# Kernel tuning notes

Hardware: AMD Instinct MI355X
Metric: run time of the kernel (lower is better)

Reference implementation:

```python
import jax, jax.numpy as jnp
import numpy as np

D_MODEL = 1024
N_HEAD = 16
D_K = D_MODEL // N_HEAD


def setup_inputs() -> dict:
    key = jax.random.key(0)
    ks = jax.random.split(key, 11)
    B, T = 2, 2048
    s = 1.0 / np.sqrt(D_MODEL)
    return {
        "q": jax.random.normal(ks[0], (B, T, D_MODEL), jnp.float32),
        "k": jax.random.normal(ks[1], (B, T, D_MODEL), jnp.float32),
        "v": jax.random.normal(ks[2], (B, T, D_MODEL), jnp.float32),
        "w_q": jax.random.normal(ks[3], (D_MODEL, D_MODEL), jnp.float32) * s,
        "b_q": jax.random.normal(ks[4], (D_MODEL,), jnp.float32) * 0.01,
        "w_k": jax.random.normal(ks[5], (D_MODEL, D_MODEL), jnp.float32) * s,
        "b_k": jax.random.normal(ks[6], (D_MODEL,), jnp.float32) * 0.01,
        "w_v": jax.random.normal(ks[7], (D_MODEL, D_MODEL), jnp.float32) * s,
        "b_v": jax.random.normal(ks[8], (D_MODEL,), jnp.float32) * 0.01,
        "w_o": jax.random.normal(ks[9], (D_MODEL, D_MODEL), jnp.float32) * s,
        "b_o": jax.random.normal(ks[10], (D_MODEL,), jnp.float32) * 0.01,
    }


def reference(q, k, v, w_q, b_q, w_k, b_k, w_v, b_v, w_o, b_o):
    B, T, _ = q.shape
    # QKV projections -> [B, H, T, d_k]
    def proj(x, w, b):
        return (jnp.einsum('btd,de->bte', x, w) + b).reshape(B, T, N_HEAD, D_K).transpose(0, 2, 1, 3)
    qh = proj(q, w_q, b_q)
    kh = proj(k, w_k, b_k)
    vh = proj(v, w_v, b_v)
    scale = jnp.float32(1.0 / np.sqrt(D_K))
    scores = jnp.einsum('bhqd,bhkd->bhqk', qh, kh) * scale  # [B,H,T,T]
    attn = jax.nn.softmax(scores, axis=-1)
    # dropout is identity in eval mode
    out = jnp.einsum('bhqk,bhkd->bhqd', attn, vh)  # [B,H,T,d_k]
    out = out.transpose(0, 2, 1, 3).reshape(B, T, N_HEAD * D_K)
    return jnp.einsum('btd,de->bte', out, w_o) + b_o
```

## Files before the change

kernel.cpp:

```cpp
#include <hip/hip_runtime.h>
#include <stdint.h>

#define DEVI static __device__ __forceinline__

typedef float f32x4 __attribute__((ext_vector_type(4)));
typedef float f32x16 __attribute__((ext_vector_type(16)));
typedef short s16x8 __attribute__((ext_vector_type(8)));
typedef unsigned short u16x4 __attribute__((ext_vector_type(4)));
typedef uint32_t u32x2 __attribute__((ext_vector_type(2)));
typedef uint32_t u32x4 __attribute__((ext_vector_type(4)));

DEVI unsigned short f2bf(float f) {
  union { float f; uint32_t u; } v; v.f = f;
  uint32_t u = v.u;
  return (unsigned short)((u + 0x7fffu + ((u >> 16) & 1u)) >> 16);
}

DEVI uint32_t cvtpk(float lo, float hi) {
  uint32_t r;
  asm("v_cvt_pk_bf16_f32 %0, %1, %2" : "=v"(r) : "v"(lo), "v"(hi));
  return r;
}

DEVI void pl32swap(uint32_t& a, uint32_t& b) {
#if __has_builtin(__builtin_amdgcn_permlane32_swap)
  u32x2 r = __builtin_amdgcn_permlane32_swap(a, b, false, false);
  a = r[0]; b = r[1];
#else
  asm("v_permlane32_swap_b32 %0, %1" : "+v"(a), "+v"(b));
#endif
}

DEVI float swap_half(float x, int hi) {
  uint32_t a = __float_as_uint(x), b = a;
  pl32swap(a, b);
  return hi ? __uint_as_float(a) : __uint_as_float(b);
}

DEVI void g2l16(const void* g, void* l) {
  __builtin_amdgcn_global_load_lds(
      (const __attribute__((address_space(1))) void*)g,
      (__attribute__((address_space(3))) void*)l, 16, 0, 0);
}

DEVI float vmax16(const f32x16& v) {
  float a = fmaxf(fmaxf(v[0], v[1]), fmaxf(v[2], v[3]));
  float b = fmaxf(fmaxf(v[4], v[5]), fmaxf(v[6], v[7]));
  float c = fmaxf(fmaxf(v[8], v[9]), fmaxf(v[10], v[11]));
  float d = fmaxf(fmaxf(v[12], v[13]), fmaxf(v[14], v[15]));
  return fmaxf(fmaxf(a, b), fmaxf(c, d));
}

DEVI float vsum16(const f32x16& v) {
  float a = (v[0] + v[1]) + (v[2] + v[3]);
  float b = (v[4] + v[5]) + (v[6] + v[7]);
  float c = (v[8] + v[9]) + (v[10] + v[11]);
  float d = (v[12] + v[13]) + (v[14] + v[15]);
  return (a + b) + (c + d);
}

__global__ __launch_bounds__(256) void k_cvt3(const float* __restrict__ q,
                                              const float* __restrict__ k,
                                              const float* __restrict__ v,
                                              unsigned short* __restrict__ out) {
  const int y = blockIdx.y;
  const float* in = y == 0 ? q : y == 1 ? k : v;
  unsigned short* o = out + (size_t)y * 4194304;
  int idx = blockIdx.x * blockDim.x + threadIdx.x;
  int stride = gridDim.x * blockDim.x;
  for (int i = idx * 4; i < 4194304; i += stride * 4) {
    f32x4 x = *(const f32x4*)(in + i);
    u16x4 r;
    for (int j = 0; j < 4; ++j) r[j] = f2bf(x[j]);
    *(u16x4*)(o + i) = r;
  }
}

__global__ __launch_bounds__(256) void k_wt4(const float* w0, const float* w1,
                                             const float* w2, const float* w3,
                                             unsigned short* t0, unsigned short* t1,
                                             unsigned short* t2, unsigned short* t3) {
  const int z = blockIdx.z;
  const float* w = z == 0 ? w0 : z == 1 ? w1 : z == 2 ? w2 : w3;
  unsigned short* wt = z == 0 ? t0 : z == 1 ? t1 : z == 2 ? t2 : t3;
  __shared__ float tile[32][33];
  const int tx = threadIdx.x, ty = threadIdx.y;
  const int n0 = blockIdx.x * 32, k0 = blockIdx.y * 32;
  for (int j = 0; j < 4; ++j)
    tile[ty + j * 8][tx] = w[(size_t)(k0 + ty + j * 8) * 1024 + n0 + tx];
  __syncthreads();
  for (int j = 0; j < 4; ++j)
    wt[(size_t)(n0 + ty + j * 8) * 1024 + k0 + tx] = f2bf(tile[tx][ty + j * 8]);
}

__global__ __launch_bounds__(256) void k_gemm_multi(
    const unsigned short* A0, const unsigned short* A1, const unsigned short* A2,
    const unsigned short* B0, const unsigned short* B1, const unsigned short* B2,
    const float* c0, const float* c1, const float* c2,
    void* o0, void* o1, void* o2, int mode0) {
  constexpr int K = 1024;
  const int z = blockIdx.y;
  const unsigned short* A = z == 0 ? A0 : z == 1 ? A1 : A2;
  const unsigned short* Bt = z == 0 ? B0 : z == 1 ? B1 : B2;
  const float* bias = z == 0 ? c0 : z == 1 ? c1 : c2;
  void* outp = z == 0 ? o0 : z == 1 ? o1 : o2;
  const int MODE = mode0 + z;

  __shared__ __align__(16) unsigned short As[128 * 64];
  __shared__ __align__(16) unsigned short Bs[64 * 64];
  const int tid = threadIdx.x;
  const int lane = tid & 63, w = tid >> 6;
  const int g = lane >> 4, c = lane & 15;
  const int wgid = (blockIdx.x & 7) * 64 + (blockIdx.x >> 3);
  const int bm = wgid >> 4, bn = wgid & 15;
  const int m0 = bm * 128, n0 = bn * 64;
  const int wr = w >> 1, wc = w & 1;
  f32x4 acc[4][2] = {};

  for (int kt = 0; kt < 16; ++kt) {
    const int k0 = kt * 64;
    __syncthreads();
#pragma unroll
    for (int it = 0; it < 4; ++it) {
      int e = it * 256 + tid;
      int row = e >> 3, cwp = (e & 7) ^ (row & 7);
      g2l16(A + (size_t)(m0 + row) * K + k0 + cwp * 8,
            (char*)As + (it * 256 + (w << 6)) * 16);
    }
#pragma unroll
    for (int it = 0; it < 2; ++it) {
      int e = it * 256 + tid;
      int row = e >> 3, cwp = (e & 7) ^ (row & 7);
      g2l16(Bt + (size_t)(n0 + row) * K + k0 + cwp * 8,
            (char*)Bs + (it * 256 + (w << 6)) * 16);
    }
    __syncthreads();
    for (int kk = 0; kk < 2; ++kk) {
      s16x8 af[4], bfr[2];
      for (int mi = 0; mi < 4; ++mi) {
        int row = wr * 64 + mi * 16 + c;
        int ch = (kk * 4 + g) ^ (row & 7);
        af[mi] = *(const s16x8*)((const char*)As + row * 128 + ch * 16);
      }
      for (int ni = 0; ni < 2; ++ni) {
        int row = wc * 32 + ni * 16 + c;
        int ch = (kk * 4 + g) ^ (row & 7);
        bfr[ni] = *(const s16x8*)((const char*)Bs + row * 128 + ch * 16);
      }
      for (int mi = 0; mi < 4; ++mi)
        for (int ni = 0; ni < 2; ++ni)
          acc[mi][ni] = __builtin_amdgcn_mfma_f32_16x16x32_bf16(
              af[mi], bfr[ni], acc[mi][ni], 0, 0, 0);
    }
  }

  if (MODE == 0 || MODE == 1) {
    unsigned short* out = (unsigned short*)outp;
    const float scale = (MODE == 0) ? 0.1803368801111204f : 1.0f;
    for (int mi = 0; mi < 4; ++mi)
      for (int ni = 0; ni < 2; ++ni) {
        int row = m0 + wr * 64 + mi * 16 + g * 4;
        int col = n0 + wc * 32 + ni * 16 + c;
        float bb = bias[col];
        for (int r = 0; r < 4; ++r)
          out[(size_t)(row + r) * 1024 + col] = f2bf((acc[mi][ni][r] + bb) * scale);
      }
  } else if (MODE == 2) {
    unsigned short* vt = (unsigned short*)outp;
    const int bq = m0 >> 11, t0 = m0 & 2047;
    for (int mi = 0; mi < 4; ++mi)
      for (int ni = 0; ni < 2; ++ni) {
        int rowb = wr * 64 + mi * 16 + g * 4;
        int coll = wc * 32 + ni * 16 + c;
        float bb = bias[n0 + coll];
        u16x4 pk;
        for (int r = 0; r < 4; ++r) pk[r] = f2bf(acc[mi][ni][r] + bb);
        *(u16x4*)(vt + (size_t)(bq * 1024 + n0 + coll) * 2048 + t0 + rowb) = pk;
      }
  } else {
    float* out = (float*)outp;
    for (int mi = 0; mi < 4; ++mi)
      for (int ni = 0; ni < 2; ++ni) {
        int row = m0 + wr * 64 + mi * 16 + g * 4;
        int col = n0 + wc * 32 + ni * 16 + c;
        float bb = bias[col];
        for (int r = 0; r < 4; ++r)
          out[(size_t)(row + r) * 1024 + col] = acc[mi][ni][r] + bb;
      }
  }
}

__global__ __launch_bounds__(128) void k_attn(const unsigned short* __restrict__ Qp,
                                              const unsigned short* __restrict__ Kp,
                                              const unsigned short* __restrict__ Vt,
                                              unsigned short* __restrict__ Att) {
  __shared__ __align__(16) unsigned short Ks[2][4096];
  __shared__ __align__(16) unsigned short Vs[2][4096];
  const int tid = threadIdx.x;
  const int lane = tid & 63, w = tid >> 6;
  const int l31 = lane & 31, hi = lane >> 5;
  const int blk = (blockIdx.x & 7) * 128 + (blockIdx.x >> 3);
  const int qt = blk & 31, bh = blk >> 5;
  const int b = bh >> 4, h = bh & 15;
  const int m0 = qt * 64 + w * 32;
  const size_t qkBase = (size_t)b * 2048 * 1024 + (size_t)h * 64;
  const size_t vtBase = ((size_t)b * 1024 + h * 64) * 2048;

  const unsigned short* qrow = Qp + qkBase + (size_t)(m0 + l31) * 1024;
  s16x8 bq[4];
#pragma unroll
  for (int s = 0; s < 4; ++s)
    bq[s] = *(const s16x8*)(qrow + s * 16 + hi * 8);

  const int srow = tid >> 1, half = tid & 1;
  const unsigned short* kg = Kp + qkBase + (size_t)srow * 1024 + half * 32;
  const unsigned short* vg = Vt + vtBase + (size_t)srow * 2048 + half * 32;
  int wof[4];
#pragma unroll
  for (int j = 0; j < 4; ++j)
    wof[j] = srow * 128 + (((half * 4 + j) ^ (srow & 7)) * 16);

  float m_run = -1e30f, l_run = 0.f;
  f32x16 o0 = {}, o1 = {};

  {
    s16x8 k0 = *(const s16x8*)(kg), k1 = *(const s16x8*)(kg + 8);
    s16x8 k2 = *(const s16x8*)(kg + 16), k3 = *(const s16x8*)(kg + 24);
    s16x8 v0 = *(const s16x8*)(vg), v1 = *(const s16x8*)(vg + 8);
    s16x8 v2 = *(const s16x8*)(vg + 16), v3 = *(const s16x8*)(vg + 24);
    *(s16x8*)((char*)&Ks[0][0] + wof[0]) = k0;
    *(s16x8*)((char*)&Ks[0][0] + wof[1]) = k1;
    *(s16x8*)((char*)&Ks[0][0] + wof[2]) = k2;
    *(s16x8*)((char*)&Ks[0][0] + wof[3]) = k3;
    *(s16x8*)((char*)&Vs[0][0] + wof[0]) = v0;
    *(s16x8*)((char*)&Vs[0][0] + wof[1]) = v1;
    *(s16x8*)((char*)&Vs[0][0] + wof[2]) = v2;
    *(s16x8*)((char*)&Vs[0][0] + wof[3]) = v3;
  }
  __syncthreads();

  const int rch = l31 & 7;

#pragma unroll 1
  for (int t = 0; t < 32; ++t) {
    const int cur = t & 1;
    s16x8 k0, k1, k2, k3, v0, v1, v2, v3;
    if (t < 31) {
      const unsigned short* kgt = kg + (size_t)(t + 1) * 65536;
      const unsigned short* vgt = vg + (t + 1) * 64;
      k0 = *(const s16x8*)(kgt);      k1 = *(const s16x8*)(kgt + 8);
      k2 = *(const s16x8*)(kgt + 16); k3 = *(const s16x8*)(kgt + 24);
      v0 = *(const s16x8*)(vgt);      v1 = *(const s16x8*)(vgt + 8);
      v2 = *(const s16x8*)(vgt + 16); v3 = *(const s16x8*)(vgt + 24);
    }
    const char* ks = (const char*)&Ks[cur][0];
    const char* vs = (const char*)&Vs[cur][0];

    f32x16 s0 = {}, s1 = {};
    __builtin_amdgcn_s_setprio(1);
#pragma unroll
    for (int ds = 0; ds < 4; ++ds) {
      int ch = (2 * ds + hi) ^ rch;
      s16x8 a0 = *(const s16x8*)(ks + l31 * 128 + ch * 16);
      s16x8 a1 = *(const s16x8*)(ks + (32 + l31) * 128 + ch * 16);
      s0 = __builtin_amdgcn_mfma_f32_32x32x16_bf16(a0, bq[ds], s0, 0, 0, 0);
      s1 = __builtin_amdgcn_mfma_f32_32x32x16_bf16(a1, bq[ds], s1, 0, 0, 0);
    }
    __builtin_amdgcn_s_setprio(0);

    float tm = fmaxf(vmax16(s0), vmax16(s1));
    tm = fmaxf(tm, swap_half(tm, hi));
    if (!__all(tm - m_run <= 8.0f)) {
      float mt = fmaxf(m_run, tm);
      float al = exp2f(m_run - mt);
      l_run *= al;
#pragma unroll
      for (int j = 0; j < 16; ++j) { o0[j] *= al; o1[j] *= al; }
      m_run = mt;
    }
#pragma unroll
    for (int j = 0; j < 16; ++j) s0[j] = exp2f(s0[j] - m_run);
#pragma unroll
    for (int j = 0; j < 16; ++j) s1[j] = exp2f(s1[j] - m_run);
    l_run += vsum16(s0) + vsum16(s1);

    s16x8 pf[4];
    {
      uint32_t w0 = cvtpk(s0[0], s0[1]), w1 = cvtpk(s0[2], s0[3]);
      uint32_t w2 = cvtpk(s0[4], s0[5]), w3 = cvtpk(s0[6], s0[7]);
      uint32_t w4 = cvtpk(s0[8], s0[9]), w5 = cvtpk(s0[10], s0[11]);
      uint32_t w6 = cvtpk(s0[12], s0[13]), w7 = cvtpk(s0[14], s0[15]);
      pl32swap(w0, w2); pl32swap(w1, w3); pl32swap(w4, w6); pl32swap(w5, w7);
      u32x4 f0 = {w0, w1, w2, w3}, f1 = {w4, w5, w6, w7};
      pf[0] = *(s16x8*)&f0;
      pf[1] = *(s16x8*)&f1;
    }
    {
      uint32_t w0 = cvtpk(s1[0], s1[1]), w1 = cvtpk(s1[2], s1[3]);
      uint32_t w2 = cvtpk(s1[4], s1[5]), w3 = cvtpk(s1[6], s1[7]);
      uint32_t w4 = cvtpk(s1[8], s1[9]), w5 = cvtpk(s1[10], s1[11]);
      uint32_t w6 = cvtpk(s1[12], s1[13]), w7 = cvtpk(s1[14], s1[15]);
      pl32swap(w0, w2); pl32swap(w1, w3); pl32swap(w4, w6); pl32swap(w5, w7);
      u32x4 f0 = {w0, w1, w2, w3}, f1 = {w4, w5, w6, w7};
      pf[2] = *(s16x8*)&f0;
      pf[3] = *(s16x8*)&f1;
    }

    __builtin_amdgcn_s_setprio(1);
#pragma unroll
    for (int ksp = 0; ksp < 4; ++ksp) {
      int ch = (2 * ksp + hi) ^ rch;
      s16x8 a0 = *(const s16x8*)(vs + l31 * 128 + ch * 16);
      s16x8 a1 = *(const s16x8*)(vs + (32 + l31) * 128 + ch * 16);
      o0 = __builtin_amdgcn_mfma_f32_32x32x16_bf16(a0, pf[ksp], o0, 0, 0, 0);
      o1 = __builtin_amdgcn_mfma_f32_32x32x16_bf16(a1, pf[ksp], o1, 0, 0, 0);
    }
    __builtin_amdgcn_s_setprio(0);

    if (t < 31) {
      const int nb = cur ^ 1;
      *(s16x8*)((char*)&Ks[nb][0] + wof[0]) = k0;
      *(s16x8*)((char*)&Ks[nb][0] + wof[1]) = k1;
      *(s16x8*)((char*)&Ks[nb][0] + wof[2]) = k2;
      *(s16x8*)((char*)&Ks[nb][0] + wof[3]) = k3;
      *(s16x8*)((char*)&Vs[nb][0] + wof[0]) = v0;
      *(s16x8*)((char*)&Vs[nb][0] + wof[1]) = v1;
      *(s16x8*)((char*)&Vs[nb][0] + wof[2]) = v2;
      *(s16x8*)((char*)&Vs[nb][0] + wof[3]) = v3;
    }
    __syncthreads();
  }

  float lt = l_run + swap_half(l_run, hi);
  float inv = 1.0f / lt;
  unsigned short* arow = Att + ((size_t)b * 2048 + m0 + l31) * 1024 + h * 64;
#pragma unroll
  for (int dblk = 0; dblk < 2; ++dblk) {
#pragma unroll
    for (int rq = 0; rq < 4; ++rq) {
      float e0 = (dblk ? o1[rq * 4 + 0] : o0[rq * 4 + 0]) * inv;
      float e1 = (dblk ? o1[rq * 4 + 1] : o0[rq * 4 + 1]) * inv;
      float e2 = (dblk ? o1[rq * 4 + 2] : o0[rq * 4 + 2]) * inv;
      float e3 = (dblk ? o1[rq * 4 + 3] : o0[rq * 4 + 3]) * inv;
      u32x2 pk;
      pk[0] = cvtpk(e0, e1);
      pk[1] = cvtpk(e2, e3);
      *(u32x2*)(arow + dblk * 32 + 8 * rq + 4 * hi) = pk;
    }
  }
}

extern "C" void kernel_launch(void* const* d_in, const int* in_sizes, int n_in,
                              void* d_out, int out_size, void* d_ws, size_t ws_size,
                              hipStream_t stream) {
  const float* q = (const float*)d_in[0];
  const float* k = (const float*)d_in[1];
  const float* v = (const float*)d_in[2];
  const float* w_q = (const float*)d_in[3];
  const float* b_q = (const float*)d_in[4];
  const float* w_k = (const float*)d_in[5];
  const float* b_k = (const float*)d_in[6];
  const float* w_v = (const float*)d_in[7];
  const float* b_v = (const float*)d_in[8];
  const float* w_o = (const float*)d_in[9];
  const float* b_o = (const float*)d_in[10];

  unsigned short* s = (unsigned short*)d_ws;
  unsigned short* qbf = s;
  unsigned short* kbf = s + 4194304;
  unsigned short* vbf = s + 8388608;
  unsigned short* wqT = s + 12582912;
  unsigned short* wkT = s + 13631488;
  unsigned short* wvT = s + 14680064;
  unsigned short* woT = s + 15728640;
  unsigned short* Qp  = s + 16777216;
  unsigned short* Kp  = s + 20971520;
  unsigned short* Vt  = s + 25165824;
  unsigned short* Att = qbf;

  k_cvt3<<<dim3(1024, 3), 256, 0, stream>>>(q, k, v, qbf);

  k_wt4<<<dim3(32, 32, 4), dim3(32, 8), 0, stream>>>(w_q, w_k, w_v, w_o,
                                                     wqT, wkT, wvT, woT);

  k_gemm_multi<<<dim3(512, 3), 256, 0, stream>>>(
      qbf, kbf, vbf, wqT, wkT, wvT, b_q, b_k, b_v,
      (void*)Qp, (void*)Kp, (void*)Vt, 0);

  k_attn<<<1024, 128, 0, stream>>>(Qp, Kp, Vt, Att);

  k_gemm_multi<<<dim3(512, 1), 256, 0, stream>>>(
      Att, Att, Att, woT, woT, woT, b_o, b_o, b_o,
      d_out, d_out, d_out, 3);
}
```

Before: 147.3 us.

## Split attention over two key halves with 128-query blocks and a combine kernel

The attention kernel now uses 256-thread blocks covering 128 queries, so four waves share each K/V tile loaded into LDS. Each block processes only half of the key sequence. Per-half normalized outputs and (max, sum) statistics go to workspace, and a new combine kernel merges them with softmax rescaling. This is meant to improve K/V reuse per block and keep the grid size unchanged. In exchange it adds an extra launch, extra global traffic for the bf16 partial outputs, and a second bf16 rounding step. Softmax exponentials also switch to the native exp2 builtin.

```diff
diff --git a/kernel.cpp b/kernel.cpp
--- a/kernel.cpp
+++ b/kernel.cpp
@@ -16,10 +16,24 @@
   return (unsigned short)((u + 0x7fffu + ((u >> 16) & 1u)) >> 16);
 }
 
+DEVI float bf2f(unsigned short u) {
+  union { uint32_t u; float f; } v;
+  v.u = ((uint32_t)u) << 16;
+  return v.f;
+}
+
 DEVI uint32_t cvtpk(float lo, float hi) {
   uint32_t r;
   asm("v_cvt_pk_bf16_f32 %0, %1, %2" : "=v"(r) : "v"(lo), "v"(hi));
   return r;
+}
+
+DEVI float fexp2(float x) {
+#if __has_builtin(__builtin_amdgcn_exp2f)
+  return __builtin_amdgcn_exp2f(x);
+#else
+  return exp2f(x);
+#endif
 }
 
 DEVI void pl32swap(uint32_t& a, uint32_t& b) {
@@ -190,19 +204,21 @@
   }
 }
 
-__global__ __launch_bounds__(128) void k_attn(const unsigned short* __restrict__ Qp,
+__global__ __launch_bounds__(256) void k_attn(const unsigned short* __restrict__ Qp,
                                               const unsigned short* __restrict__ Kp,
                                               const unsigned short* __restrict__ Vt,
-                                              unsigned short* __restrict__ Att) {
+                                              unsigned short* __restrict__ Po0,
+                                              unsigned short* __restrict__ Po1,
+                                              float2* __restrict__ ml) {
   __shared__ __align__(16) unsigned short Ks[2][4096];
   __shared__ __align__(16) unsigned short Vs[2][4096];
   const int tid = threadIdx.x;
   const int lane = tid & 63, w = tid >> 6;
   const int l31 = lane & 31, hi = lane >> 5;
   const int blk = (blockIdx.x & 7) * 128 + (blockIdx.x >> 3);
-  const int qt = blk & 31, bh = blk >> 5;
+  const int half = blk & 1, qt = (blk >> 1) & 15, bh = blk >> 5;
   const int b = bh >> 4, h = bh & 15;
-  const int m0 = qt * 64 + w * 32;
+  const int m0 = qt * 128 + w * 32;
   const size_t qkBase = (size_t)b * 2048 * 1024 + (size_t)h * 64;
   const size_t vtBase = ((size_t)b * 1024 + h * 64) * 2048;
 
@@ -212,46 +228,40 @@
   for (int s = 0; s < 4; ++s)
     bq[s] = *(const s16x8*)(qrow + s * 16 + hi * 8);
 
-  const int srow = tid >> 1, half = tid & 1;
-  const unsigned short* kg = Kp + qkBase + (size_t)srow * 1024 + half * 32;
-  const unsigned short* vg = Vt + vtBase + (size_t)srow * 2048 + half * 32;
-  int wof[4];
-#pragma unroll
-  for (int j = 0; j < 4; ++j)
-    wof[j] = srow * 128 + (((half * 4 + j) ^ (srow & 7)) * 16);
+  const int srow = tid >> 2, c4 = tid & 3;
+  const unsigned short* kg = Kp + qkBase + (size_t)srow * 1024 + c4 * 16 +
+                             (size_t)half * 1048576;
+  const unsigned short* vg = Vt + vtBase + (size_t)srow * 2048 + c4 * 16 +
+                             half * 1024;
+  int wof[2];
+#pragma unroll
+  for (int j = 0; j < 2; ++j)
+    wof[j] = srow * 128 + (((c4 * 2 + j) ^ (srow & 7)) * 16);
 
   float m_run = -1e30f, l_run = 0.f;
   f32x16 o0 = {}, o1 = {};
 
   {
     s16x8 k0 = *(const s16x8*)(kg), k1 = *(const s16x8*)(kg + 8);
-    s16x8 k2 = *(const s16x8*)(kg + 16), k3 = *(const s16x8*)(kg + 24);
     s16x8 v0 = *(const s16x8*)(vg), v1 = *(const s16x8*)(vg + 8);
-    s16x8 v2 = *(const s16x8*)(vg + 16), v3 = *(const s16x8*)(vg + 24);
     *(s16x8*)((char*)&Ks[0][0] + wof[0]) = k0;
     *(s16x8*)((char*)&Ks[0][0] + wof[1]) = k1;
-    *(s16x8*)((char*)&Ks[0][0] + wof[2]) = k2;
-    *(s16x8*)((char*)&Ks[0][0] + wof[3]) = k3;
     *(s16x8*)((char*)&Vs[0][0] + wof[0]) = v0;
     *(s16x8*)((char*)&Vs[0][0] + wof[1]) = v1;
-    *(s16x8*)((char*)&Vs[0][0] + wof[2]) = v2;
-    *(s16x8*)((char*)&Vs[0][0] + wof[3]) = v3;
   }
   __syncthreads();
 
   const int rch = l31 & 7;
 
 #pragma unroll 1
-  for (int t = 0; t < 32; ++t) {
+  for (int t = 0; t < 16; ++t) {
     const int cur = t & 1;
-    s16x8 k0, k1, k2, k3, v0, v1, v2, v3;
-    if (t < 31) {
+    s16x8 k0, k1, v0, v1;
+    if (t < 15) {
       const unsigned short* kgt = kg + (size_t)(t + 1) * 65536;
       const unsigned short* vgt = vg + (t + 1) * 64;
-      k0 = *(const s16x8*)(kgt);      k1 = *(const s16x8*)(kgt + 8);
-      k2 = *(const s16x8*)(kgt + 16); k3 = *(const s16x8*)(kgt + 24);
-      v0 = *(const s16x8*)(vgt);      v1 = *(const s16x8*)(vgt + 8);
-      v2 = *(const s16x8*)(vgt + 16); v3 = *(const s16x8*)(vgt + 24);
+      k0 = *(const s16x8*)(kgt); k1 = *(const s16x8*)(kgt + 8);
+      v0 = *(const s16x8*)(vgt); v1 = *(const s16x8*)(vgt + 8);
     }
     const char* ks = (const char*)&Ks[cur][0];
     const char* vs = (const char*)&Vs[cur][0];
@@ -272,16 +282,16 @@
     tm = fmaxf(tm, swap_half(tm, hi));
     if (!__all(tm - m_run <= 8.0f)) {
       float mt = fmaxf(m_run, tm);
-      float al = exp2f(m_run - mt);
+      float al = fexp2(m_run - mt);
       l_run *= al;
 #pragma unroll
       for (int j = 0; j < 16; ++j) { o0[j] *= al; o1[j] *= al; }
       m_run = mt;
     }
 #pragma unroll
-    for (int j = 0; j < 16; ++j) s0[j] = exp2f(s0[j] - m_run);
-#pragma unroll
-    for (int j = 0; j < 16; ++j) s1[j] = exp2f(s1[j] - m_run);
+    for (int j = 0; j < 16; ++j) s0[j] = fexp2(s0[j] - m_run);
+#pragma unroll
+    for (int j = 0; j < 16; ++j) s1[j] = fexp2(s1[j] - m_run);
     l_run += vsum16(s0) + vsum16(s1);
 
     s16x8 pf[4];
@@ -317,23 +327,20 @@
     }
     __builtin_amdgcn_s_setprio(0);
 
-    if (t < 31) {
+    if (t < 15) {
       const int nb = cur ^ 1;
       *(s16x8*)((char*)&Ks[nb][0] + wof[0]) = k0;
       *(s16x8*)((char*)&Ks[nb][0] + wof[1]) = k1;
-      *(s16x8*)((char*)&Ks[nb][0] + wof[2]) = k2;
-      *(s16x8*)((char*)&Ks[nb][0] + wof[3]) = k3;
       *(s16x8*)((char*)&Vs[nb][0] + wof[0]) = v0;
       *(s16x8*)((char*)&Vs[nb][0] + wof[1]) = v1;
-      *(s16x8*)((char*)&Vs[nb][0] + wof[2]) = v2;
-      *(s16x8*)((char*)&Vs[nb][0] + wof[3]) = v3;
     }
     __syncthreads();
   }
 
   float lt = l_run + swap_half(l_run, hi);
   float inv = 1.0f / lt;
-  unsigned short* arow = Att + ((size_t)b * 2048 + m0 + l31) * 1024 + h * 64;
+  unsigned short* Po = half ? Po1 : Po0;
+  unsigned short* arow = Po + ((size_t)b * 2048 + m0 + l31) * 1024 + h * 64;
 #pragma unroll
   for (int dblk = 0; dblk < 2; ++dblk) {
 #pragma unroll
@@ -348,6 +355,36 @@
       *(u32x2*)(arow + dblk * 32 + 8 * rq + 4 * hi) = pk;
     }
   }
+  if (hi == 0) {
+    int qid = ((b << 4) + h) * 2048 + m0 + l31;
+    ml[half * 65536 + qid] = {m_run, lt};
+  }
+}
+
+__global__ __launch_bounds__(256) void k_comb(const unsigned short* __restrict__ Po0,
+                                              const unsigned short* __restrict__ Po1,
+                                              const float2* __restrict__ ml,
+                                              unsigned short* __restrict__ Att) {
+  int idx = blockIdx.x * 256 + threadIdx.x;
+  int base = idx * 8;
+  int qrow = base >> 10, col = base & 1023;
+  int h = col >> 6, b = qrow >> 11, t = qrow & 2047;
+  int qid = ((b << 4) + h) * 2048 + t;
+  float2 p0 = ml[qid], p1 = ml[65536 + qid];
+  float ms = fmaxf(p0.x, p1.x);
+  float a0 = fexp2(p0.x - ms) * p0.y, a1 = fexp2(p1.x - ms) * p1.y;
+  float inv = 1.0f / (a0 + a1);
+  float w0 = a0 * inv, w1 = a1 * inv;
+  s16x8 v0 = *(const s16x8*)(Po0 + base);
+  s16x8 v1 = *(const s16x8*)(Po1 + base);
+  u32x4 pk;
+#pragma unroll
+  for (int j = 0; j < 4; ++j) {
+    float e0 = w0 * bf2f((unsigned short)v0[2 * j]) + w1 * bf2f((unsigned short)v1[2 * j]);
+    float e1 = w0 * bf2f((unsigned short)v0[2 * j + 1]) + w1 * bf2f((unsigned short)v1[2 * j + 1]);
+    pk[j] = cvtpk(e0, e1);
+  }
+  *(u32x4*)(Att + base) = pk;
 }
 
 extern "C" void kernel_launch(void* const* d_in, const int* in_sizes, int n_in,
@@ -376,7 +413,10 @@
   unsigned short* Qp  = s + 16777216;
   unsigned short* Kp  = s + 20971520;
   unsigned short* Vt  = s + 25165824;
-  unsigned short* Att = qbf;
+  unsigned short* Po0 = qbf;
+  unsigned short* Po1 = kbf;
+  unsigned short* Att = vbf;
+  float2* ml = (float2*)wqT;
 
   k_cvt3<<<dim3(1024, 3), 256, 0, stream>>>(q, k, v, qbf);
 
@@ -387,7 +427,9 @@
       qbf, kbf, vbf, wqT, wkT, wvT, b_q, b_k, b_v,
       (void*)Qp, (void*)Kp, (void*)Vt, 0);
 
-  k_attn<<<1024, 128, 0, stream>>>(Qp, Kp, Vt, Att);
+  k_attn<<<1024, 256, 0, stream>>>(Qp, Kp, Vt, Po0, Po1, ml);
+
+  k_comb<<<2048, 256, 0, stream>>>(Po0, Po1, ml, Att);
 
   k_gemm_multi<<<dim3(512, 1), 256, 0, stream>>>(
       Att, Att, Att, woT, woT, woT, b_o, b_o, b_o,
```

After: 134.7 us. 8.6% less time.
